# Kernel optimization log

Measured on AMD Instinct MI355X. Metric: run time of the kernel, lower is better.

Reference implementation:

```python
import jax, jax.numpy as jnp
import numpy as np

BS, S, D, H = 2, 2048, 1024, 16
DH = D // H  # 64


def setup_inputs() -> dict:
    key = jax.random.key(0)
    k1, k2, k3 = jax.random.split(key, 3)
    x = jax.random.normal(k1, (BS, S, D), dtype=jnp.float32)
    w_qkv = jax.random.normal(k2, (D, H, 3 * DH), dtype=jnp.float32) * (D ** -0.5)
    b_qkv = jnp.zeros((H, 3 * DH), dtype=jnp.float32)
    w_out = jax.random.normal(k3, (H, DH, D), dtype=jnp.float32) * (D ** -0.5)
    b_out = jnp.zeros((D,), dtype=jnp.float32)
    return {"x": x, "w_qkv": w_qkv, "b_qkv": b_qkv, "w_out": w_out, "b_out": b_out}


def reference(x, w_qkv, b_qkv, w_out, b_out):
    dtype = x.dtype
    # QKV projection: DenseGeneral(features=(H, 3*DH)) -> [B, S, H, 3*DH]
    qkv = jnp.einsum("bsd,dhf->bshf", x, w_qkv) + b_qkv
    q, k, v = jnp.split(qkv, 3, axis=-1)  # each [B, S, H, DH]

    scale = DH ** -0.5
    q = (q * scale).astype(jnp.float32)
    k = k.astype(jnp.float32)
    # Full causal attention with fp32 scores (as in original)
    weights = jnp.einsum("bqhd,bkhd->bhqk", q, k)  # [B, H, S, S]
    causal = jnp.tril(jnp.ones((S, S), dtype=bool))[None, None, :, :]
    weights = jnp.where(causal, weights, jnp.finfo(jnp.float32).min)
    weights = jax.nn.softmax(weights, axis=-1).astype(dtype)
    attn = jnp.einsum("bhqk,bkhd->bqhd", weights, v).astype(dtype)

    # Output projection: DenseGeneral(D, axis=(-2, -1))
    out = jnp.einsum("bqhd,hdo->bqo", attn, w_out) + b_out
    return out
```

## Files before the change

### kernel.cpp

```cpp
#include <hip/hip_runtime.h>
#include <hip/hip_bf16.h>
#include <stdint.h>

#define NBS 2
#define SEQ 2048
#define DMODEL 1024
#define NH 16
#define DHEAD 64
#define MROWS (NBS*SEQ)
#define NQKV (NH*3*DHEAD)

typedef __bf16 bf16;
typedef __bf16 bf16x8 __attribute__((ext_vector_type(8)));
typedef float f32x4 __attribute__((ext_vector_type(4)));
typedef float f32x16 __attribute__((ext_vector_type(16)));
typedef unsigned int u32x2 __attribute__((ext_vector_type(2)));

#define LOG2E 1.44269504088896f
#define QSCALE (0.125f * LOG2E)

static __device__ __forceinline__ void gload_lds16(const bf16* g, bf16* l) {
    __builtin_amdgcn_global_load_lds(
        (const __attribute__((address_space(1))) uint32_t*)g,
        (__attribute__((address_space(3))) uint32_t*)l, 16, 0, 0);
}

static __device__ __forceinline__ bf16x8 ld_b8(const bf16* p) {
    return __builtin_bit_cast(bf16x8, *(const uint4*)p);
}

static __device__ __forceinline__ uint32_t pk_bf16(float lo, float hi) {
    unsigned short l = __builtin_bit_cast(unsigned short, (bf16)lo);
    unsigned short h = __builtin_bit_cast(unsigned short, (bf16)hi);
    return ((uint32_t)h << 16) | (uint32_t)l;
}

static __device__ __forceinline__ u32x2 lane_swap32(uint32_t a, uint32_t b, int lane) {
#if __has_builtin(__builtin_amdgcn_permlane32_swap)
    return __builtin_amdgcn_permlane32_swap(a, b, false, false);
#else
    uint32_t sa = __shfl_xor(a, 32), sb = __shfl_xor(b, 32);
    u32x2 r;
    r.x = (lane >= 32) ? sb : a;
    r.y = (lane >= 32) ? b : sa;
    return r;
#endif
}


__global__ void k_cvt(const float* __restrict__ in, bf16* __restrict__ out, int n4) {
    int i = blockIdx.x * blockDim.x + threadIdx.x;
    if (i < n4) {
        float4 v = ((const float4*)in)[i];
        ushort4 o;
        o.x = __builtin_bit_cast(unsigned short, (bf16)v.x);
        o.y = __builtin_bit_cast(unsigned short, (bf16)v.y);
        o.z = __builtin_bit_cast(unsigned short, (bf16)v.z);
        o.w = __builtin_bit_cast(unsigned short, (bf16)v.w);
        ((ushort4*)out)[i] = o;
    }
}

__global__ void k_tcvt(const float* __restrict__ in, bf16* __restrict__ out, int R, int C) {
    __shared__ float t[32][33];
    int tx = threadIdx.x, ty = threadIdx.y;
    int r0 = blockIdx.y * 32, c0 = blockIdx.x * 32;
#pragma unroll
    for (int i = 0; i < 4; i++)
        t[ty + i*8][tx] = in[(size_t)(r0 + ty + i*8) * C + (c0 + tx)];
    __syncthreads();
#pragma unroll
    for (int i = 0; i < 4; i++)
        out[(size_t)(c0 + ty + i*8) * R + (r0 + tx)] = (bf16)t[tx][ty + i*8];
}

__global__ void k_tcvt_qkv(const float* __restrict__ in, bf16* __restrict__ out) {
    __shared__ float t[32][33];
    int tx = threadIdx.x, ty = threadIdx.y;
    int r0 = blockIdx.y * 32, c0 = blockIdx.x * 32;
#pragma unroll
    for (int i = 0; i < 4; i++)
        t[ty + i*8][tx] = in[(size_t)(r0 + ty + i*8) * NQKV + (c0 + tx)];
    __syncthreads();
#pragma unroll
    for (int i = 0; i < 4; i++) {
        int c = c0 + ty + i*8;
        int h = c / 192, f = c % 192;
        int cperm = ((f >> 6) << 10) + (h << 6) + (f & 63);
        out[(size_t)cperm * DMODEL + (r0 + tx)] = (bf16)t[tx][ty + i*8];
    }
}

template<int KD>
static __device__ __forceinline__ void gemm_tile(
        const bf16* __restrict__ A, const bf16* __restrict__ Bt,
        bf16* As, bf16* Bs, f32x4 acc[4][4], int tile_m, int tile_n) {
    int tid = threadIdx.x;
    int wave = tid >> 6, lane = tid & 63;
    int wr = wave >> 1, wc = wave & 1;
    int g = lane >> 4, r = lane & 15;
    int grow = lane >> 3;
    int gc8 = (lane & 7) ^ grow;

#pragma unroll
    for (int m = 0; m < 4; m++)
#pragma unroll
        for (int n = 0; n < 4; n++)
            acc[m][n] = (f32x4){0.f, 0.f, 0.f, 0.f};

    int sw = (r & 7) << 3;

    for (int k0 = 0; k0 < KD; k0 += 64) {
#pragma unroll
        for (int i = 0; i < 4; i++) {
            int ii = wave + i * 4;
            gload_lds16(A  + (size_t)(tile_m + ii*8 + grow) * KD + k0 + gc8*8, As + ii*512);
            gload_lds16(Bt + (size_t)(tile_n + ii*8 + grow) * KD + k0 + gc8*8, Bs + ii*512);
        }
        __syncthreads();
#pragma unroll
        for (int kk = 0; kk < 2; kk++) {
            bf16x8 af[4], bfr[4];
#pragma unroll
            for (int m = 0; m < 4; m++)
                af[m] = ld_b8(As + ((((wr*64 + m*16 + r)*64) + kk*32 + g*8) ^ sw));
#pragma unroll
            for (int n = 0; n < 4; n++)
                bfr[n] = ld_b8(Bs + ((((wc*64 + n*16 + r)*64) + kk*32 + g*8) ^ sw));
#pragma unroll
            for (int m = 0; m < 4; m++)
#pragma unroll
                for (int n = 0; n < 4; n++)
                    acc[m][n] = __builtin_amdgcn_mfma_f32_16x16x32_bf16(af[m], bfr[n], acc[m][n], 0, 0, 0);
        }
        __syncthreads();
    }
}

__global__ __launch_bounds__(256) void k_gemm_qkv(
        const bf16* __restrict__ A, const bf16* __restrict__ Bt,
        const float* __restrict__ bias,
        bf16* __restrict__ Q, bf16* __restrict__ Kp, bf16* __restrict__ Vt) {
    __shared__ __align__(16) bf16 As[128*64];
    __shared__ __align__(16) bf16 Bs[128*64];
    f32x4 acc[4][4];
    int tile_m = blockIdx.y * 128, tile_n = blockIdx.x * 128;
    gemm_tile<DMODEL>(A, Bt, As, Bs, acc, tile_m, tile_n);

    int wave = threadIdx.x >> 6, lane = threadIdx.x & 63;
    int wr = wave >> 1, wc = wave & 1, g = lane >> 4, r = lane & 15;
#pragma unroll
    for (int m = 0; m < 4; m++) {
#pragma unroll
        for (int n = 0; n < 4; n++) {
            int col = tile_n + wc*64 + n*16 + r;
            int kind = col >> 10;
            int h = (col >> 6) & 15;
            int d = col & 63;
            float bv = bias[h*192 + (kind << 6) + d];
#pragma unroll
            for (int j = 0; j < 4; j++) {
                int row = tile_m + wr*64 + m*16 + g*4 + j;
                int b = row >> 11, s = row & 2047;
                float v = acc[m][n][j] + bv;
                if (kind == 0) {
                    Q[(((size_t)(b*NH + h)) * SEQ + s) * DHEAD + d] = (bf16)(v * QSCALE);
                } else if (kind == 1) {
                    Kp[(((size_t)(b*NH + h)) * SEQ + s) * DHEAD + d] = (bf16)v;
                } else {
                    Vt[(((size_t)(b*NH + h)) * DHEAD + d) * SEQ + s] = (bf16)v;
                }
            }
        }
    }
}

__global__ __launch_bounds__(256) void k_gemm_out(
        const bf16* __restrict__ A, const bf16* __restrict__ Bt,
        const float* __restrict__ bias, float* __restrict__ out) {
    __shared__ __align__(16) bf16 As[128*64];
    __shared__ __align__(16) bf16 Bs[128*64];
    f32x4 acc[4][4];
    int tile_m = blockIdx.y * 128, tile_n = blockIdx.x * 128;
    gemm_tile<DMODEL>(A, Bt, As, Bs, acc, tile_m, tile_n);

    int wave = threadIdx.x >> 6, lane = threadIdx.x & 63;
    int wr = wave >> 1, wc = wave & 1, g = lane >> 4, r = lane & 15;
#pragma unroll
    for (int m = 0; m < 4; m++) {
#pragma unroll
        for (int n = 0; n < 4; n++) {
            int col = tile_n + wc*64 + n*16 + r;
            float bv = bias[col];
#pragma unroll
            for (int j = 0; j < 4; j++) {
                int row = tile_m + wr*64 + m*16 + g*4 + j;
                out[(size_t)row * DMODEL + col] = acc[m][n][j] + bv;
            }
        }
    }
}

#define QBLK 128
#define KVB 64

static __device__ __forceinline__ void attn_tile_body(
        const bf16* Ks, const bf16* VsT,
        const bf16x8 qa2[4], const bf16x8& ones,
        f32x16 o32[2], f32x16& acc_l,
        int kv0, int qb, int qrow, int l31, int hi, int lane) {
    const f32x16 z16 = {0,0,0,0,0,0,0,0,0,0,0,0,0,0,0,0};
    int sw = (l31 & 7) << 3;
    f32x16 st[2];
    st[0] = z16; st[1] = z16;
    __builtin_amdgcn_s_setprio(1);
#pragma unroll
    for (int rb = 0; rb < 2; rb++) {
#pragma unroll
        for (int c = 0; c < 4; c++) {
            bf16x8 kf = ld_b8(Ks + ((((rb*32 + l31)*64) + c*16 + hi*8) ^ sw));
            st[rb] = __builtin_amdgcn_mfma_f32_32x32x16_bf16(kf, qa2[c], st[rb], 0, 0, 0);
        }
    }
    __builtin_amdgcn_s_setprio(0);

    bf16x8 vf[2][4];
#pragma unroll
    for (int dblk = 0; dblk < 2; dblk++)
#pragma unroll
        for (int c = 0; c < 4; c++)
            vf[dblk][c] = ld_b8(VsT + ((((dblk*32 + l31)*64) + c*16 + hi*8) ^ sw));

    bool needm = (kv0 + KVB - 1) > qb;
#pragma unroll
    for (int rb = 0; rb < 2; rb++) {
#pragma unroll
        for (int reg = 0; reg < 16; reg++) {
            float e = __builtin_amdgcn_exp2f(st[rb][reg]);
            if (needm) {
                int kv = kv0 + rb*32 + (reg & 3) + 8*(reg >> 2) + 4*hi;
                if (kv > qrow) e = 0.f;
            }
            st[rb][reg] = e;
        }
    }

    bf16x8 pa[4];
#pragma unroll
    for (int c = 0; c < 4; c++) {
        const f32x16& pp = st[c >> 1];
        const int base = (c & 1) * 8;
        uint32_t a0 = pk_bf16(pp[base+0], pp[base+1]);
        uint32_t a1 = pk_bf16(pp[base+2], pp[base+3]);
        uint32_t b0 = pk_bf16(pp[base+4], pp[base+5]);
        uint32_t b1 = pk_bf16(pp[base+6], pp[base+7]);
        u32x2 s0 = lane_swap32(a0, b0, lane);
        u32x2 s1 = lane_swap32(a1, b1, lane);
        uint4 fr = {s0.x, s1.x, s0.y, s1.y};
        pa[c] = __builtin_bit_cast(bf16x8, fr);
    }

    __builtin_amdgcn_s_setprio(1);
#pragma unroll
    for (int dblk = 0; dblk < 2; dblk++)
#pragma unroll
        for (int c = 0; c < 4; c++)
            o32[dblk] = __builtin_amdgcn_mfma_f32_32x32x16_bf16(pa[c], vf[dblk][c], o32[dblk], 0, 0, 0);
#pragma unroll
    for (int c = 0; c < 4; c++)
        acc_l = __builtin_amdgcn_mfma_f32_32x32x16_bf16(pa[c], ones, acc_l, 0, 0, 0);
    __builtin_amdgcn_s_setprio(0);
}

__device__ const int8_t JQC[32]  = {10,10, 4, 0, 15,15, 3, 1,  9, 9, 7, 2, 13,14, 7, 5,
                                    14,14,11, 5, 15, 8,11, 6,  8,12,12, 6, 13,13,11,12};
__device__ const int8_t JT0[32]  = { 0,11, 0, 0,  0,11, 0, 0,  0,10, 0, 0,  0, 0, 8, 0,
                                    10,20, 0, 6, 22, 0, 8, 0,  9, 0, 9, 7, 10,19,16,18};
__device__ const int8_t JT1[32]  = {11,22,10, 2, 11,22, 8, 4, 10,20, 8, 6, 10,10,16, 6,
                                    20,30, 8,12, 32, 9,16, 7, 18, 9,18,14, 19,28,24,26};
__device__ const int8_t JSEG[32] = { 0, 1, 0, 0,  0, 1, 0, 0,  0, 1, 0, 0,  0, 0, 1, 0,
                                     1, 2, 0, 1,  2, 0, 1, 0,  1, 0, 1, 1,  1, 2, 2, 2};

__global__ __launch_bounds__(256) void k_attn_split(
        const bf16* __restrict__ Q, const bf16* __restrict__ K,
        const bf16* __restrict__ Vt,
        bf16* __restrict__ Op0, bf16* __restrict__ Op1, bf16* __restrict__ Op2,
        float* __restrict__ Lp0, float* __restrict__ Lp1, float* __restrict__ Lp2) {
    int scu = blockIdx.x;
    int bh = scu >> 3, slot = scu & 7;
    int j = slot * 4 + blockIdx.y;
    int qc  = JQC[j];
    int t0  = JT0[j];
    int t1  = JT1[j];
    int seg = JSEG[j];
    int q0 = qc * QBLK;
    int tid = threadIdx.x, wave = tid >> 6, lane = tid & 63;
    int l31 = lane & 31, hi = lane >> 5;

    __shared__ __align__(16) bf16 Ks[2][KVB*64];
    __shared__ __align__(16) bf16 VsT[2][KVB*64];

    const bf16* Kg = K  + (size_t)bh * SEQ * DHEAD;
    const bf16* Vg = Vt + (size_t)bh * DHEAD * SEQ;

    int qb = q0 + wave * 32;
    int qrow = qb + l31;

    const bf16* qrow_p = Q + ((size_t)bh * SEQ + qrow) * DHEAD;
    bf16x8 qa2[4];
#pragma unroll
    for (int c = 0; c < 4; c++) qa2[c] = ld_b8(qrow_p + c*16 + hi*8);

    bf16x8 ones;
#pragma unroll
    for (int c = 0; c < 8; c++) ones[c] = (bf16)1.0f;

    const f32x16 z16 = {0,0,0,0,0,0,0,0,0,0,0,0,0,0,0,0};
    f32x16 o32[2], acc_l;
    o32[0] = z16; o32[1] = z16; acc_l = z16;

    int qmax_wave = qb + 31;

    int srow = tid >> 3, sc8 = tid & 7;
    int sw_st = (srow & 7) << 3;
    int wK0 = ((srow*64)      + sc8*8) ^ sw_st;
    int wK1 = (((srow+32)*64) + sc8*8) ^ sw_st;

    bf16x8 kreg[2], vreg[2];
    {
        int kvs = t0 * KVB;
        kreg[0] = ld_b8(Kg + (size_t)(kvs + srow)      * DHEAD + sc8*8);
        kreg[1] = ld_b8(Kg + (size_t)(kvs + srow + 32) * DHEAD + sc8*8);
        vreg[0] = ld_b8(Vg + (size_t)srow      * SEQ + kvs + sc8*8);
        vreg[1] = ld_b8(Vg + (size_t)(srow+32) * SEQ + kvs + sc8*8);
    }

    int cur = 0;
    for (int t = t0; t < t1; t++) {
        int kv0 = t * KVB;
        *(uint4*)&Ks[cur][wK0]  = __builtin_bit_cast(uint4, kreg[0]);
        *(uint4*)&Ks[cur][wK1]  = __builtin_bit_cast(uint4, kreg[1]);
        *(uint4*)&VsT[cur][wK0] = __builtin_bit_cast(uint4, vreg[0]);
        *(uint4*)&VsT[cur][wK1] = __builtin_bit_cast(uint4, vreg[1]);
        __syncthreads();

        if (t + 1 < t1) {
            int kv1 = kv0 + KVB;
            kreg[0] = ld_b8(Kg + (size_t)(kv1 + srow)      * DHEAD + sc8*8);
            kreg[1] = ld_b8(Kg + (size_t)(kv1 + srow + 32) * DHEAD + sc8*8);
            vreg[0] = ld_b8(Vg + (size_t)srow      * SEQ + kv1 + sc8*8);
            vreg[1] = ld_b8(Vg + (size_t)(srow+32) * SEQ + kv1 + sc8*8);
        }

        if (kv0 <= qmax_wave)
            attn_tile_body(Ks[cur], VsT[cur], qa2, ones, o32, acc_l,
                           kv0, qb, qrow, l31, hi, lane);
        cur ^= 1;
    }

    bf16* Op; float* Lp; size_t obase; int lbase;
    if (seg == 0)      { Op = Op0; Lp = Lp0; obase = ((size_t)bh*2048 + q0) * 64;          lbase = bh*2048 + q0; }
    else if (seg == 1) { Op = Op1; Lp = Lp1; obase = ((size_t)bh*1408 + (qc-5)*128) * 64;  lbase = bh*1408 + (qc-5)*128; }
    else               { Op = Op2; Lp = Lp2; obase = ((size_t)bh*640  + (qc-11)*128) * 64; lbase = bh*640  + (qc-11)*128; }

    if (l31 == 0) {
#pragma unroll
        for (int reg = 0; reg < 16; reg++) {
            int qr = (reg & 3) + 8*(reg >> 2) + 4*hi;
            Lp[lbase + wave*32 + qr] = acc_l[reg];
        }
    }

#pragma unroll
    for (int reg = 0; reg < 16; reg++) {
        int qr = (reg & 3) + 8*(reg >> 2) + 4*hi;
        size_t base = obase + (size_t)(wave*32 + qr) * 64 + l31;
        Op[base]      = (bf16)o32[0][reg];
        Op[base + 32] = (bf16)o32[1][reg];
    }
}

__global__ __launch_bounds__(256) void k_merge(
        const bf16* __restrict__ Op0, const bf16* __restrict__ Op1,
        const bf16* __restrict__ Op2,
        const float* __restrict__ Lp0, const float* __restrict__ Lp1,
        const float* __restrict__ Lp2,
        bf16* __restrict__ Oa) {
    int g = blockIdx.x * 256 + threadIdx.x;
    int dseg = g & 7;
    int s = (g >> 3) & 2047;
    int bh = g >> 14;
    int qc = s >> 7;
    int sl = s & 127;

    size_t r0 = ((size_t)bh * 2048 + s) * 64 + dseg*8;
    bf16x8 p0 = ld_b8(Op0 + r0);
    float l = Lp0[bh*2048 + s];
    float acc[8];
#pragma unroll
    for (int i = 0; i < 8; i++) acc[i] = (float)p0[i];

    if (qc >= 5) {
        size_t r1 = ((size_t)bh * 1408 + (qc-5)*128 + sl) * 64 + dseg*8;
        bf16x8 p1 = ld_b8(Op1 + r1);
        l += Lp1[bh*1408 + (qc-5)*128 + sl];
#pragma unroll
        for (int i = 0; i < 8; i++) acc[i] += (float)p1[i];
        if (qc >= 11) {
            size_t r2 = ((size_t)bh * 640 + (qc-11)*128 + sl) * 64 + dseg*8;
            bf16x8 p2 = ld_b8(Op2 + r2);
            l += Lp2[bh*640 + (qc-11)*128 + sl];
#pragma unroll
            for (int i = 0; i < 8; i++) acc[i] += (float)p2[i];
        }
    }

    float inv = 1.0f / l;
    bf16x8 r;
#pragma unroll
    for (int i = 0; i < 8; i++) r[i] = (bf16)(acc[i] * inv);
    int b = bh >> 4, h = bh & 15;
    *(uint4*)&Oa[(((size_t)b * SEQ + s) * NH + h) * DHEAD + dseg*8] =
        __builtin_bit_cast(uint4, r);
}

__global__ __launch_bounds__(256) void k_attn(
        const bf16* __restrict__ Q, const bf16* __restrict__ K,
        const bf16* __restrict__ Vt, bf16* __restrict__ O) {
    int bh = blockIdx.y;
    int qc = (bh >= 16) ? (15 - (int)blockIdx.x) : (int)blockIdx.x;
    int q0 = qc * QBLK;
    int tid = threadIdx.x, wave = tid >> 6, lane = tid & 63;
    int l31 = lane & 31, hi = lane >> 5;

    __shared__ __align__(16) bf16 Ks[2][KVB*64];
    __shared__ __align__(16) bf16 VsT[2][KVB*64];

    const bf16* Kg = K  + (size_t)bh * SEQ * DHEAD;
    const bf16* Vg = Vt + (size_t)bh * DHEAD * SEQ;

    int qb = q0 + wave * 32;
    int qrow = qb + l31;

    const bf16* qrow_p = Q + ((size_t)bh * SEQ + qrow) * DHEAD;
    bf16x8 qa2[4];
#pragma unroll
    for (int c = 0; c < 4; c++) qa2[c] = ld_b8(qrow_p + c*16 + hi*8);

    bf16x8 ones;
#pragma unroll
    for (int c = 0; c < 8; c++) ones[c] = (bf16)1.0f;

    const f32x16 z16 = {0,0,0,0,0,0,0,0,0,0,0,0,0,0,0,0};
    f32x16 o32[2], acc_l;
    o32[0] = z16; o32[1] = z16; acc_l = z16;

    int nt = 2*qc + 2;
    int qmax_wave = qb + 31;

    int srow = tid >> 3, sc8 = tid & 7;
    int sw_st = (srow & 7) << 3;
    int wK0 = ((srow*64)      + sc8*8) ^ sw_st;
    int wK1 = (((srow+32)*64) + sc8*8) ^ sw_st;

    bf16x8 kreg[2], vreg[2];
    kreg[0] = ld_b8(Kg + (size_t)srow      * DHEAD + sc8*8);
    kreg[1] = ld_b8(Kg + (size_t)(srow+32) * DHEAD + sc8*8);
    vreg[0] = ld_b8(Vg + (size_t)srow      * SEQ + sc8*8);
    vreg[1] = ld_b8(Vg + (size_t)(srow+32) * SEQ + sc8*8);

    int cur = 0;
    for (int t = 0; t < nt; t++) {
        int kv0 = t * KVB;
        *(uint4*)&Ks[cur][wK0]  = __builtin_bit_cast(uint4, kreg[0]);
        *(uint4*)&Ks[cur][wK1]  = __builtin_bit_cast(uint4, kreg[1]);
        *(uint4*)&VsT[cur][wK0] = __builtin_bit_cast(uint4, vreg[0]);
        *(uint4*)&VsT[cur][wK1] = __builtin_bit_cast(uint4, vreg[1]);
        __syncthreads();

        if (t + 1 < nt) {
            int kv1 = kv0 + KVB;
            kreg[0] = ld_b8(Kg + (size_t)(kv1 + srow)      * DHEAD + sc8*8);
            kreg[1] = ld_b8(Kg + (size_t)(kv1 + srow + 32) * DHEAD + sc8*8);
            vreg[0] = ld_b8(Vg + (size_t)srow      * SEQ + kv1 + sc8*8);
            vreg[1] = ld_b8(Vg + (size_t)(srow+32) * SEQ + kv1 + sc8*8);
        }

        if (kv0 <= qmax_wave)
            attn_tile_body(Ks[cur], VsT[cur], qa2, ones, o32, acc_l,
                           kv0, qb, qrow, l31, hi, lane);
        cur ^= 1;
    }

    int b = bh >> 4, h = bh & 15;
#pragma unroll
    for (int reg = 0; reg < 16; reg++) {
        int qr = (reg & 3) + 8*(reg >> 2) + 4*hi;
        int srow2 = q0 + wave*32 + qr;
        float linv = 1.0f / acc_l[reg];
        size_t base = (((size_t)b * SEQ + srow2) * NH + h) * DHEAD + l31;
        O[base]      = (bf16)(o32[0][reg] * linv);
        O[base + 32] = (bf16)(o32[1][reg] * linv);
    }
}


extern "C" void kernel_launch(void* const* d_in, const int* in_sizes, int n_in,
                              void* d_out, int out_size, void* d_ws, size_t ws_size,
                              hipStream_t stream) {
    const float* x     = (const float*)d_in[0];
    const float* w_qkv = (const float*)d_in[1];
    const float* b_qkv = (const float*)d_in[2];
    const float* w_out = (const float*)d_in[3];
    const float* b_out = (const float*)d_in[4];
    float* out = (float*)d_out;

    char* ws = (char*)d_ws;
    bf16* xb   = (bf16*)(ws);
    bf16* wqkT = (bf16*)(ws + 8388608);
    bf16* woT  = (bf16*)(ws + 14680064);
    bf16* qb   = (bf16*)(ws + 16777216);
    bf16* kb   = (bf16*)(ws + 25165824);
    bf16* vb   = (bf16*)(ws + 33554432);
    bf16* Op0  = (bf16*)(ws + 41943040);
    bf16* Op1  = (bf16*)(ws + 50331648);
    bf16* Op2  = (bf16*)(ws + 56098816);
    float* Lp0 = (float*)(ws + 8388608);
    float* Lp1 = (float*)(ws + 8388608 + 262144);
    float* Lp2 = (float*)(ws + 8388608 + 524288);
    const size_t WS_NEED = 58720256;
    bf16* attn = xb;

    k_cvt<<<(MROWS*DMODEL/4 + 255)/256, 256, 0, stream>>>(x, xb, MROWS*DMODEL/4);
    dim3 tb(32, 8);
    k_tcvt_qkv<<<dim3(NQKV/32, DMODEL/32), tb, 0, stream>>>(w_qkv, wqkT);
    k_tcvt<<<dim3(DMODEL/32, DMODEL/32), tb, 0, stream>>>(w_out, woT, DMODEL, DMODEL);

    k_gemm_qkv<<<dim3(NQKV/128, MROWS/128), 256, 0, stream>>>(xb, wqkT, b_qkv, qb, kb, vb);

    if (ws_size >= WS_NEED) {
        k_attn_split<<<dim3(256, 4), 256, 0, stream>>>(qb, kb, vb,
                                                       Op0, Op1, Op2, Lp0, Lp1, Lp2);
        k_merge<<<(NBS*NH*SEQ*DHEAD/8)/256, 256, 0, stream>>>(Op0, Op1, Op2,
                                                              Lp0, Lp1, Lp2, attn);
    } else {
        k_attn<<<dim3(SEQ/QBLK, NBS*NH), 256, 0, stream>>>(qb, kb, vb, attn);
    }

    k_gemm_out<<<dim3(DMODEL/128, MROWS/128), 256, 0, stream>>>(attn, woT, b_out, out);
}
```

Measured before the change: 140.8 us.

## Shrink GEMM K-step to 32, drop LDS swizzle, use 64x128 tiles for out-proj

```diff
diff --git a/kernel.cpp b/kernel.cpp
--- a/kernel.cpp
+++ b/kernel.cpp
@@ -99,8 +99,7 @@
     int wave = tid >> 6, lane = tid & 63;
     int wr = wave >> 1, wc = wave & 1;
     int g = lane >> 4, r = lane & 15;
-    int grow = lane >> 3;
-    int gc8 = (lane & 7) ^ grow;
+    int srow = lane >> 2, schunk = (lane & 3) * 8;
 
 #pragma unroll
     for (int m = 0; m < 4; m++)
@@ -108,31 +107,24 @@
         for (int n = 0; n < 4; n++)
             acc[m][n] = (f32x4){0.f, 0.f, 0.f, 0.f};
 
-    int sw = (r & 7) << 3;
-
-    for (int k0 = 0; k0 < KD; k0 += 64) {
-#pragma unroll
-        for (int i = 0; i < 4; i++) {
+    for (int k0 = 0; k0 < KD; k0 += 32) {
+#pragma unroll
+        for (int i = 0; i < 2; i++) {
             int ii = wave + i * 4;
-            gload_lds16(A  + (size_t)(tile_m + ii*8 + grow) * KD + k0 + gc8*8, As + ii*512);
-            gload_lds16(Bt + (size_t)(tile_n + ii*8 + grow) * KD + k0 + gc8*8, Bs + ii*512);
+            gload_lds16(A  + (size_t)(tile_m + ii*16 + srow) * KD + k0 + schunk, As + ii*512);
+            gload_lds16(Bt + (size_t)(tile_n + ii*16 + srow) * KD + k0 + schunk, Bs + ii*512);
         }
         __syncthreads();
-#pragma unroll
-        for (int kk = 0; kk < 2; kk++) {
-            bf16x8 af[4], bfr[4];
-#pragma unroll
-            for (int m = 0; m < 4; m++)
-                af[m] = ld_b8(As + ((((wr*64 + m*16 + r)*64) + kk*32 + g*8) ^ sw));
+        bf16x8 af[4], bfr[4];
+#pragma unroll
+        for (int m = 0; m < 4; m++) af[m]  = *(const bf16x8*)(As + (wr*64 + m*16 + r)*32 + g*8);
+#pragma unroll
+        for (int n = 0; n < 4; n++) bfr[n] = *(const bf16x8*)(Bs + (wc*64 + n*16 + r)*32 + g*8);
+#pragma unroll
+        for (int m = 0; m < 4; m++)
 #pragma unroll
             for (int n = 0; n < 4; n++)
-                bfr[n] = ld_b8(Bs + ((((wc*64 + n*16 + r)*64) + kk*32 + g*8) ^ sw));
-#pragma unroll
-            for (int m = 0; m < 4; m++)
-#pragma unroll
-                for (int n = 0; n < 4; n++)
-                    acc[m][n] = __builtin_amdgcn_mfma_f32_16x16x32_bf16(af[m], bfr[n], acc[m][n], 0, 0, 0);
-        }
+                acc[m][n] = __builtin_amdgcn_mfma_f32_16x16x32_bf16(af[m], bfr[n], acc[m][n], 0, 0, 0);
         __syncthreads();
     }
 }
@@ -141,8 +133,8 @@
         const bf16* __restrict__ A, const bf16* __restrict__ Bt,
         const float* __restrict__ bias,
         bf16* __restrict__ Q, bf16* __restrict__ Kp, bf16* __restrict__ Vt) {
-    __shared__ __align__(16) bf16 As[128*64];
-    __shared__ __align__(16) bf16 Bs[128*64];
+    __shared__ __align__(16) bf16 As[128*32];
+    __shared__ __align__(16) bf16 Bs[128*32];
     f32x4 acc[4][4];
     int tile_m = blockIdx.y * 128, tile_n = blockIdx.x * 128;
     gemm_tile<DMODEL>(A, Bt, As, Bs, acc, tile_m, tile_n);
@@ -178,23 +170,48 @@
 __global__ __launch_bounds__(256) void k_gemm_out(
         const bf16* __restrict__ A, const bf16* __restrict__ Bt,
         const float* __restrict__ bias, float* __restrict__ out) {
-    __shared__ __align__(16) bf16 As[128*64];
-    __shared__ __align__(16) bf16 Bs[128*64];
-    f32x4 acc[4][4];
-    int tile_m = blockIdx.y * 128, tile_n = blockIdx.x * 128;
-    gemm_tile<DMODEL>(A, Bt, As, Bs, acc, tile_m, tile_n);
-
-    int wave = threadIdx.x >> 6, lane = threadIdx.x & 63;
-    int wr = wave >> 1, wc = wave & 1, g = lane >> 4, r = lane & 15;
+    __shared__ __align__(16) bf16 As[64*32];
+    __shared__ __align__(16) bf16 Bs[128*32];
+    int tid = threadIdx.x;
+    int wave = tid >> 6, lane = tid & 63;
+    int g = lane >> 4, r = lane & 15;
+    int srow = lane >> 2, schunk = (lane & 3) * 8;
+    int tile_m = blockIdx.y * 64, tile_n = blockIdx.x * 128;
+
+    f32x4 acc[4][2];
+#pragma unroll
+    for (int m = 0; m < 4; m++)
+#pragma unroll
+        for (int n = 0; n < 2; n++)
+            acc[m][n] = (f32x4){0.f, 0.f, 0.f, 0.f};
+
+    for (int k0 = 0; k0 < DMODEL; k0 += 32) {
+        gload_lds16(A  + (size_t)(tile_m + wave*16 + srow) * DMODEL + k0 + schunk, As + wave*512);
+        gload_lds16(Bt + (size_t)(tile_n + wave*16 + srow) * DMODEL + k0 + schunk, Bs + wave*512);
+        gload_lds16(Bt + (size_t)(tile_n + 64 + wave*16 + srow) * DMODEL + k0 + schunk, Bs + 2048 + wave*512);
+        __syncthreads();
+        bf16x8 af[4], bfr[2];
+#pragma unroll
+        for (int m = 0; m < 4; m++) af[m]  = *(const bf16x8*)(As + (m*16 + r)*32 + g*8);
+#pragma unroll
+        for (int n = 0; n < 2; n++) bfr[n] = *(const bf16x8*)(Bs + (wave*32 + n*16 + r)*32 + g*8);
+#pragma unroll
+        for (int m = 0; m < 4; m++)
+#pragma unroll
+            for (int n = 0; n < 2; n++)
+                acc[m][n] = __builtin_amdgcn_mfma_f32_16x16x32_bf16(af[m], bfr[n], acc[m][n], 0, 0, 0);
+        __syncthreads();
+    }
+
 #pragma unroll
     for (int m = 0; m < 4; m++) {
 #pragma unroll
-        for (int n = 0; n < 4; n++) {
-            int col = tile_n + wc*64 + n*16 + r;
+        for (int n = 0; n < 2; n++) {
+            int col = tile_n + wave*32 + n*16 + r;
             float bv = bias[col];
 #pragma unroll
             for (int j = 0; j < 4; j++) {
-                int row = tile_m + wr*64 + m*16 + g*4 + j;
+                int row = tile_m + m*16 + g*4 + j;
                 out[(size_t)row * DMODEL + col] = acc[m][n][j] + bv;
             }
         }
@@ -547,5 +564,5 @@
         k_attn<<<dim3(SEQ/QBLK, NBS*NH), 256, 0, stream>>>(qb, kb, vb, attn);
     }
 
-    k_gemm_out<<<dim3(DMODEL/128, MROWS/128), 256, 0, stream>>>(attn, woT, b_out, out);
-}
+    k_gemm_out<<<dim3(DMODEL/128, MROWS/64), 256, 0, stream>>>(attn, woT, b_out, out);
+}
```

Result: faster. 123.2 us (-12.5%).
